# Kernel tuning notes

Hardware: AMD Instinct MI355X
Metric: run time of the kernel (lower is better)

Reference implementation:

```python
import jax, jax.numpy as jnp
import numpy as np

DIM = 128
HEADS = 4
DH = 32
SCALE = DH ** -0.5


def _ln(x, g, b):
    m = x.mean(-1, keepdims=True)
    v = x.var(-1, keepdims=True)
    return (x - m) / jnp.sqrt(v + 1e-5) * g + b


def setup_inputs() -> dict:
    key = jax.random.key(0)
    ks = jax.random.split(key, 16)
    B, N, H, W, HK, WK = 2, 6, 48, 48, 24, 24
    d, hd = DIM, HEADS * DH
    p = lambda k, s: (jax.random.normal(k, s, jnp.float32) * 0.02)
    return {
        "q": jax.random.normal(ks[0], (B, N, d, H, W), jnp.float32),
        "k": jax.random.normal(ks[1], (B, N, d, HK, WK), jnp.float32),
        "v": jax.random.normal(ks[2], (B, N, d, HK, WK), jnp.float32),
        "skip": jax.random.normal(ks[3], (B, d, H, W), jnp.float32),
        "lnq_g": jnp.ones(d), "lnq_b": jnp.zeros(d),
        "Wq": p(ks[4], (d, hd)), "bq": jnp.zeros(hd),
        "lnk_g": jnp.ones(d), "lnk_b": jnp.zeros(d),
        "Wk": p(ks[5], (d, hd)), "bk": jnp.zeros(hd),
        "lnv_g": jnp.ones(d), "lnv_b": jnp.zeros(d),
        "Wv": p(ks[6], (d, hd)), "bv": jnp.zeros(hd),
        "Wp": p(ks[7], (hd, d)), "bp": jnp.zeros(d),
        "pre_g": jnp.ones(d), "pre_b": jnp.zeros(d),
        "W1": p(ks[8], (d, 2 * d)), "b1": jnp.zeros(2 * d),
        "W2": p(ks[9], (2 * d, d)), "b2": jnp.zeros(d),
        "post_g": jnp.ones(d), "post_b": jnp.zeros(d),
    }


def reference(q, k, v, skip, lnq_g, lnq_b, Wq, bq, lnk_g, lnk_b, Wk, bk,
              lnv_g, lnv_b, Wv, bv, Wp, bp, pre_g, pre_b, W1, b1, W2, b2,
              post_g, post_b):
    B, N, d, H, W = q.shape
    _, _, _, HK, WK = k.shape
    Q, K = H * W, HK * WK
    # b n d H W -> b n (H W) d
    qx = q.transpose(0, 1, 3, 4, 2).reshape(B, N, Q, d)
    kx = k.transpose(0, 1, 3, 4, 2).reshape(B, N, K, d)
    vx = v.transpose(0, 1, 3, 4, 2).reshape(B, N * K, d)
    # norm + linear projections
    qp = _ln(qx, lnq_g, lnq_b) @ Wq + bq  # (B,N,Q,HEADS*DH)
    kp = _ln(kx, lnk_g, lnk_b) @ Wk + bk
    vp = _ln(vx, lnv_g, lnv_b) @ Wv + bv  # (B,N*K,HEADS*DH)
    # split heads: b ... (m d) -> (b m) ... d
    qp = qp.reshape(B, N, Q, HEADS, DH).transpose(0, 3, 1, 2, 4).reshape(B * HEADS, N, Q, DH)
    kp = kp.reshape(B, N, K, HEADS, DH).transpose(0, 3, 1, 2, 4).reshape(B * HEADS, N, K, DH)
    vp = vp.reshape(B, N * K, HEADS, DH).transpose(0, 2, 1, 3).reshape(B * HEADS, N * K, DH)
    # per-view scores, then softmax jointly over (n K)
    scores = SCALE * jnp.einsum('bnqd,bnkd->bnqk', qp, kp)
    scores = scores.transpose(0, 2, 1, 3).reshape(B * HEADS, Q, N * K)
    a = jax.nn.softmax(scores, axis=-1)
    out = jnp.einsum('bqk,bkd->bqd', a, vp)  # (B*HEADS, Q, DH)
    # merge heads: (b m) Q d -> b Q (m d)
    z = out.reshape(B, HEADS, Q, DH).transpose(0, 2, 1, 3).reshape(B, Q, HEADS * DH)
    z = z @ Wp + bp
    z = z + skip.transpose(0, 2, 3, 1).reshape(B, Q, d)
    z = _ln(z, pre_g, pre_b)
    z = z + (jax.nn.gelu(z @ W1 + b1, approximate=False) @ W2 + b2)
    z = _ln(z, post_g, post_b)
    return z.reshape(B, H, W, d).transpose(0, 3, 1, 2)
```

## Files before the change

### kernel.cpp

```cpp
#include <hip/hip_runtime.h>
#include <cmath>

#define B_    2
#define N_    6
#define D_    128
#define Q_    2304
#define K_    576
#define NK_   3456
#define HEADS_ 4
#define DH_   32
#define SCALE_ 0.17677669529663687f

typedef __attribute__((ext_vector_type(8))) short bf16x8;
typedef __attribute__((ext_vector_type(4))) float f32x4;

#if defined(__has_builtin)
#if __has_builtin(__builtin_amdgcn_cvt_pk_bf16_f32)
#define HAS_PK_BF16 1
#endif
#endif

static __device__ __forceinline__ unsigned short f2bf(float f) {
  union { float f; unsigned u; } x; x.f = f;
  unsigned u = x.u + 0x7fffu + ((x.u >> 16) & 1u);
  return (unsigned short)(u >> 16);
}
static __device__ __forceinline__ unsigned pkbf(float a, float b) {
#ifdef HAS_PK_BF16
  typedef __attribute__((ext_vector_type(2))) __bf16 vbf2;
  union { vbf2 v; unsigned u; } cv;
  cv.v = __builtin_amdgcn_cvt_pk_bf16_f32(a, b);
  return cv.u;
#else
  return (unsigned)f2bf(a) | ((unsigned)f2bf(b) << 16);
#endif
}

__global__ __launch_bounds__(256) void k_prep_wt(
    const float* __restrict__ Wq, const float* __restrict__ Wk,
    const float* __restrict__ Wv, const float* __restrict__ Wp,
    const float* __restrict__ W1, const float* __restrict__ W2,
    unsigned short* __restrict__ WTq, unsigned short* __restrict__ WTk,
    unsigned short* __restrict__ WTv, unsigned short* __restrict__ WTp,
    unsigned short* __restrict__ WT1, unsigned short* __restrict__ WT2)
{
  __shared__ float tile[32][33];
  const int wb = blockIdx.x, t = threadIdx.x;
  const float* src; unsigned short* dst; int Kd, J, tl;
  if      (wb < 16) { src = Wq; dst = WTq; Kd = 128; J = 128; tl = wb; }
  else if (wb < 32) { src = Wk; dst = WTk; Kd = 128; J = 128; tl = wb - 16; }
  else if (wb < 48) { src = Wv; dst = WTv; Kd = 128; J = 128; tl = wb - 32; }
  else if (wb < 64) { src = Wp; dst = WTp; Kd = 128; J = 128; tl = wb - 48; }
  else if (wb < 96) { src = W1; dst = WT1; Kd = 128; J = 256; tl = wb - 64; }
  else              { src = W2; dst = WT2; Kd = 256; J = 128; tl = wb - 96; }
  const int njt = J >> 5;
  const int tj = tl % njt, tk = tl / njt;
#pragma unroll
  for (int i = 0; i < 4; ++i) {
    int idx = t + 256 * i;
    int r = idx >> 5, c = idx & 31;
    tile[r][c] = src[(size_t)(tk * 32 + r) * J + tj * 32 + c];
  }
  __syncthreads();
#pragma unroll
  for (int i = 0; i < 2; ++i) {
    int idx = t + 256 * i;
    int rr = idx >> 4, c2 = (idx & 15) << 1;
    *(unsigned*)&dst[(size_t)(tj * 32 + rr) * Kd + tk * 32 + c2] =
        pkbf(tile[c2][rr], tile[c2 + 1][rr]);
  }
}

__global__ __launch_bounds__(256) void k_ln_proj_all(
    const float* __restrict__ qin, const float* __restrict__ kin,
    const float* __restrict__ vin,
    const float* __restrict__ lnq_g, const float* __restrict__ lnq_b,
    const float* __restrict__ lnk_g, const float* __restrict__ lnk_b,
    const float* __restrict__ lnv_g, const float* __restrict__ lnv_b,
    const unsigned short* __restrict__ WTq, const unsigned short* __restrict__ WTk,
    const unsigned short* __restrict__ WTv,
    const float* __restrict__ bq, const float* __restrict__ bk,
    const float* __restrict__ bv,
    unsigned short* __restrict__ QPh, unsigned short* __restrict__ KPh,
    unsigned short* __restrict__ VPTh)
{
  __shared__ float xs[32][132];
  __shared__ unsigned short xh[32][136];
  __shared__ float gs[128], bs[128];
  __shared__ float mu[32], rsd[32];
  const int t = threadIdx.x;
  const int bid = blockIdx.x;

  const float* x; const unsigned short* WT; const float* g; const float* bl;
  const float* bias; int S, blk, mode; float osc;
  if (bid < 864)       { mode = 0; blk = bid;        x = qin; WT = WTq; g = lnq_g; bl = lnq_b; bias = bq; S = Q_; osc = SCALE_; }
  else if (bid < 1080) { mode = 0; blk = bid - 864;  x = kin; WT = WTk; g = lnk_g; bl = lnk_b; bias = bk; S = K_; osc = 1.0f; }
  else                 { mode = 1; blk = bid - 1080; x = vin; WT = WTv; g = lnv_g; bl = lnv_b; bias = bv; S = K_; osc = 1.0f; }
  const int ntile = S >> 5;
  const int o  = blk / ntile;
  const int s0 = (blk % ntile) << 5;

  if (t < 128) { gs[t] = g[t]; bs[t] = bl[t]; }
  const float* xb = x + (size_t)o * 128 * (size_t)S + s0;
#pragma unroll
  for (int i = 0; i < 4; ++i) {
    int idx = t + 256 * i;
    int c = idx >> 3, s4 = (idx & 7) << 2;
    float4 xv = *(const float4*)&xb[(size_t)c * S + s4];
    xs[s4 + 0][c] = xv.x; xs[s4 + 1][c] = xv.y;
    xs[s4 + 2][c] = xv.z; xs[s4 + 3][c] = xv.w;
  }
  __syncthreads();
  {
    int s = t >> 3, l8 = t & 7;
    float sum = 0.f, sq = 0.f;
    for (int c = l8; c < 128; c += 8) { float v = xs[s][c]; sum += v; sq += v * v; }
#pragma unroll
    for (int off = 4; off > 0; off >>= 1) {
      sum += __shfl_down(sum, off, 8);
      sq  += __shfl_down(sq,  off, 8);
    }
    if (l8 == 0) {
      float mth = sum * 0.0078125f;
      float var = sq * 0.0078125f - mth * mth;
      mu[s] = mth; rsd[s] = rsqrtf(var + 1e-5f);
    }
  }
  __syncthreads();
#pragma unroll
  for (int i = 0; i < 8; ++i) {
    int idx = t + 256 * i;
    int s = idx >> 6, c2 = (idx & 63) << 1;
    float y0 = (xs[s][c2]     - mu[s]) * rsd[s] * gs[c2]     + bs[c2];
    float y1 = (xs[s][c2 + 1] - mu[s]) * rsd[s] * gs[c2 + 1] + bs[c2 + 1];
    *(unsigned*)&xh[s][c2] = pkbf(y0, y1);
  }
  __syncthreads();
  const int w = t >> 6, lane = t & 63, quad = lane >> 4, l16 = lane & 15;
  const f32x4 zf = {0.f, 0.f, 0.f, 0.f};
  f32x4 acc[2][2] = {{zf, zf}, {zf, zf}};
#pragma unroll
  for (int kc = 0; kc < 4; ++kc) {
    bf16x8 a0 = *(const bf16x8*)&xh[l16][kc * 32 + quad * 8];
    bf16x8 a1 = *(const bf16x8*)&xh[16 + l16][kc * 32 + quad * 8];
    bf16x8 b0 = *(const bf16x8*)&WT[(size_t)(w * 32 + l16) * 128 + kc * 32 + quad * 8];
    bf16x8 b1 = *(const bf16x8*)&WT[(size_t)(w * 32 + 16 + l16) * 128 + kc * 32 + quad * 8];
    acc[0][0] = __builtin_amdgcn_mfma_f32_16x16x32_bf16(a0, b0, acc[0][0], 0, 0, 0);
    acc[0][1] = __builtin_amdgcn_mfma_f32_16x16x32_bf16(a0, b1, acc[0][1], 0, 0, 0);
    acc[1][0] = __builtin_amdgcn_mfma_f32_16x16x32_bf16(a1, b0, acc[1][0], 0, 0, 0);
    acc[1][1] = __builtin_amdgcn_mfma_f32_16x16x32_bf16(a1, b1, acc[1][1], 0, 0, 0);
  }
  if (mode == 0) {
    unsigned short* outh = (bid < 864) ? QPh : KPh;
    __syncthreads();
#pragma unroll
    for (int mt = 0; mt < 2; ++mt)
#pragma unroll
      for (int nt = 0; nt < 2; ++nt) {
        int col = w * 32 + nt * 16 + l16;
        float bc = bias[col];
#pragma unroll
        for (int r = 0; r < 4; ++r)
          xh[mt * 16 + quad * 4 + r][col] = f2bf((acc[mt][nt][r] + bc) * osc);
      }
    __syncthreads();
#pragma unroll
    for (int i = 0; i < 2; ++i) {
      int s = i * 16 + (t >> 4), c8 = (t & 15) << 3;
      *(uint4*)&outh[((size_t)o * S + s0 + s) * 128 + c8] = *(uint4*)&xh[s][c8];
    }
  } else {
    const int b = o / 6, n = o % 6;
#pragma unroll
    for (int mt = 0; mt < 2; ++mt)
#pragma unroll
      for (int nt = 0; nt < 2; ++nt) {
        int col = w * 32 + nt * 16 + l16;
        int hh = col >> 5, dh = col & 31;
        float bc = bias[col];
        ushort4 pk;
        *(unsigned*)&pk.x = pkbf(acc[mt][nt][0] + bc, acc[mt][nt][1] + bc);
        *(unsigned*)&pk.z = pkbf(acc[mt][nt][2] + bc, acc[mt][nt][3] + bc);
        int s = n * 576 + s0 + mt * 16 + quad * 4;
        *(ushort4*)&VPTh[((size_t)(b * 4 + hh) * 32 + dh) * (size_t)NK_ + s] = pk;
      }
  }
}

__global__ __launch_bounds__(256) void k_attn_mfma(
    const unsigned short* __restrict__ QPh, const unsigned short* __restrict__ KPh,
    const unsigned short* __restrict__ VPTh, float* __restrict__ PO,
    float* __restrict__ Pl)
{
  __shared__ __align__(16) char smem_u[10240];
  unsigned short (*plds)[2][16][40] = (unsigned short (*)[2][16][40])smem_u;
  float (*ol)[16][32] = (float (*)[16][32])smem_u;
  __shared__ float ll[4][2][4][16];
  const int t = threadIdx.x;
  const int w = t >> 6, lane = t & 63;
  const int quad = lane >> 4, l16 = lane & 15;
  const int qt = blockIdx.x % 72;
  const int rest = blockIdx.x / 72;
  const int bhx = rest >> 1, ks = rest & 1;
  const int bb = bhx >> 2, h = bhx & 3;
  const int q0 = qt << 5;

  const unsigned short* vbase = VPTh + (size_t)bhx * 32 * (size_t)NK_;
  const f32x4 zf = {0.f, 0.f, 0.f, 0.f};
  f32x4 o00 = zf, o01 = zf, o10 = zf, o11 = zf;
  float lsum0 = 0.f, lsum1 = 0.f;

  const int m8 = ks * 4 + w;
  int c0 = (108 * m8) >> 3, c1 = (108 * (m8 + 1)) >> 3;

  while (c0 < c1) {
    const int nn = c0 / 18;
    const int cend = min(c1, (nn + 1) * 18);
    const unsigned short* kb = &KPh[((size_t)(bb * 6 + nn) * K_) * 128 + h * 32];
    const unsigned short* qb = &QPh[((size_t)(bb * 6 + nn) * Q_ + q0) * 128 + h * 32];
    bf16x8 qc0 = *(const bf16x8*)&qb[(size_t)l16 * 128 + quad * 8];
    bf16x8 qc1 = *(const bf16x8*)&qb[(size_t)(16 + l16) * 128 + quad * 8];

    int kl = (c0 - nn * 18) << 5;
    bf16x8 kf0 = *(const bf16x8*)&kb[(size_t)(kl + l16) * 128 + quad * 8];
    bf16x8 kf1 = *(const bf16x8*)&kb[(size_t)(kl + 16 + l16) * 128 + quad * 8];
    const unsigned short* vb = vbase + ((size_t)c0 << 5);
    bf16x8 vf0 = *(const bf16x8*)&vb[(size_t)l16 * NK_ + quad * 8];
    bf16x8 vf1 = *(const bf16x8*)&vb[(size_t)(16 + l16) * NK_ + quad * 8];

    for (int kc = c0; kc < cend; ++kc) {
      const int kln = (kc + 1 - nn * 18) << 5;
      bf16x8 nk0 = *(const bf16x8*)&kb[(size_t)(kln + l16) * 128 + quad * 8];
      bf16x8 nk1 = *(const bf16x8*)&kb[(size_t)(kln + 16 + l16) * 128 + quad * 8];
      const unsigned short* vbn = vbase + ((size_t)(kc + 1) << 5);
      bf16x8 nv0 = *(const bf16x8*)&vbn[(size_t)l16 * NK_ + quad * 8];
      bf16x8 nv1 = *(const bf16x8*)&vbn[(size_t)(16 + l16) * NK_ + quad * 8];

      f32x4 s00 = __builtin_amdgcn_mfma_f32_16x16x32_bf16(kf0, qc0, zf, 0, 0, 0);
      f32x4 s01 = __builtin_amdgcn_mfma_f32_16x16x32_bf16(kf1, qc0, zf, 0, 0, 0);
      f32x4 s10 = __builtin_amdgcn_mfma_f32_16x16x32_bf16(kf0, qc1, zf, 0, 0, 0);
      f32x4 s11 = __builtin_amdgcn_mfma_f32_16x16x32_bf16(kf1, qc1, zf, 0, 0, 0);

      float a00 = __expf(fminf(s00.x, 70.f)), a01 = __expf(fminf(s00.y, 70.f));
      float a02 = __expf(fminf(s00.z, 70.f)), a03 = __expf(fminf(s00.w, 70.f));
      float a10 = __expf(fminf(s01.x, 70.f)), a11 = __expf(fminf(s01.y, 70.f));
      float a12 = __expf(fminf(s01.z, 70.f)), a13 = __expf(fminf(s01.w, 70.f));
      lsum0 += (a00 + a01 + a02 + a03) + (a10 + a11 + a12 + a13);
      float b00 = __expf(fminf(s10.x, 70.f)), b01 = __expf(fminf(s10.y, 70.f));
      float b02 = __expf(fminf(s10.z, 70.f)), b03 = __expf(fminf(s10.w, 70.f));
      float b10 = __expf(fminf(s11.x, 70.f)), b11 = __expf(fminf(s11.y, 70.f));
      float b12 = __expf(fminf(s11.z, 70.f)), b13 = __expf(fminf(s11.w, 70.f));
      lsum1 += (b00 + b01 + b02 + b03) + (b10 + b11 + b12 + b13);

      uint2 w0a; w0a.x = pkbf(a00, a01); w0a.y = pkbf(a02, a03);
      uint2 w0b; w0b.x = pkbf(a10, a11); w0b.y = pkbf(a12, a13);
      uint2 w1a; w1a.x = pkbf(b00, b01); w1a.y = pkbf(b02, b03);
      uint2 w1b; w1b.x = pkbf(b10, b11); w1b.y = pkbf(b12, b13);
      *(uint2*)&plds[w][0][l16][quad * 4]      = w0a;
      *(uint2*)&plds[w][0][l16][16 + quad * 4] = w0b;
      *(uint2*)&plds[w][1][l16][quad * 4]      = w1a;
      *(uint2*)&plds[w][1][l16][16 + quad * 4] = w1b;
      bf16x8 pf0 = *(const bf16x8*)&plds[w][0][l16][quad * 8];
      bf16x8 pf1 = *(const bf16x8*)&plds[w][1][l16][quad * 8];

      o00 = __builtin_amdgcn_mfma_f32_16x16x32_bf16(pf0, vf0, o00, 0, 0, 0);
      o01 = __builtin_amdgcn_mfma_f32_16x16x32_bf16(pf0, vf1, o01, 0, 0, 0);
      o10 = __builtin_amdgcn_mfma_f32_16x16x32_bf16(pf1, vf0, o10, 0, 0, 0);
      o11 = __builtin_amdgcn_mfma_f32_16x16x32_bf16(pf1, vf1, o11, 0, 0, 0);

      kf0 = nk0; kf1 = nk1; vf0 = nv0; vf1 = nv1;
    }
    c0 = cend;
  }

  ll[w][0][quad][l16] = lsum0;
  ll[w][1][quad][l16] = lsum1;
#pragma unroll
  for (int tt = 0; tt < 2; ++tt) {
    __syncthreads();
    f32x4 t0 = tt ? o10 : o00;
    f32x4 t1 = tt ? o11 : o01;
#pragma unroll
    for (int r = 0; r < 4; ++r) {
      ol[w][quad * 4 + r][l16]      = t0[r];
      ol[w][quad * 4 + r][16 + l16] = t1[r];
    }
    __syncthreads();
    const int q = t >> 4, i16 = t & 15, dd = i16 << 1;
    float a0 = 0.f, a1 = 0.f;
#pragma unroll
    for (int ww = 0; ww < 4; ++ww) { a0 += ol[ww][q][dd]; a1 += ol[ww][q][dd + 1]; }
    float2 r2; r2.x = a0; r2.y = a1;
    *(float2*)&PO[(((size_t)ks * 8 + bhx) * Q_ + q0 + tt * 16 + q) * 32 + dd] = r2;
    if (i16 == 0) {
      float l = 0.f;
#pragma unroll
      for (int ww = 0; ww < 4; ++ww)
#pragma unroll
        for (int qq = 0; qq < 4; ++qq) l += ll[ww][tt][qq][q];
      Pl[((size_t)ks * 8 + bhx) * Q_ + q0 + tt * 16 + q] = l;
    }
  }
}

__global__ __launch_bounds__(512) void k_tail(
    const float* __restrict__ PO, const float* __restrict__ Pl,
    const unsigned short* __restrict__ WTp, const float* __restrict__ bp,
    const float* __restrict__ skip,
    const float* __restrict__ pre_g, const float* __restrict__ pre_b,
    const unsigned short* __restrict__ WT1, const float* __restrict__ b1,
    const unsigned short* __restrict__ WT2, const float* __restrict__ b2,
    const float* __restrict__ post_g, const float* __restrict__ post_b,
    float* __restrict__ out)
{
  __shared__ float xs[16][132];
  __shared__ unsigned short xh[16][136];
  __shared__ unsigned short hb[16][264];
  __shared__ float g1s[128], b1s[128], g2s[128], b2s[128];
  __shared__ float mu[16], rsd[16];
  const int t = threadIdx.x;
  const int row0 = blockIdx.x << 4;
  const int bb = row0 / Q_, hw0 = row0 % Q_;
  const int w = t >> 6, lane = t & 63, quad = lane >> 4, l16 = lane & 15;
  const f32x4 zf = {0.f, 0.f, 0.f, 0.f};

  if (t < 128) { g1s[t] = pre_g[t]; b1s[t] = pre_b[t]; g2s[t] = post_g[t]; b2s[t] = post_b[t]; }
#pragma unroll
  for (int i = 0; i < 2; ++i) {
    int idx = t + 512 * i;
    int s = idx >> 6, c2 = (idx & 63) << 1;
    int q = hw0 + s;
    int h = c2 >> 5, dh = c2 & 31;
    size_t bq = (size_t)(bb * 4 + h) * Q_ + q;
    size_t i0 = bq * 32 + dh;
    float2 p0 = *(const float2*)&PO[i0];
    float2 p1 = *(const float2*)&PO[589824 + i0];
    float inv = 1.f / (Pl[bq] + Pl[18432 + bq]);
    *(unsigned*)&xh[s][c2] = pkbf((p0.x + p1.x) * inv, (p0.y + p1.y) * inv);
  }
  __syncthreads();
  {
    f32x4 acc = zf;
    const int col = w * 16 + l16;
#pragma unroll
    for (int kc = 0; kc < 4; ++kc) {
      bf16x8 a0 = *(const bf16x8*)&xh[l16][kc * 32 + quad * 8];
      bf16x8 b0 = *(const bf16x8*)&WTp[(size_t)col * 128 + kc * 32 + quad * 8];
      acc = __builtin_amdgcn_mfma_f32_16x16x32_bf16(a0, b0, acc, 0, 0, 0);
    }
    float bc = bp[col];
    float4 sk = *(const float4*)&skip[((size_t)bb * 128 + col) * Q_ + hw0 + quad * 4];
    xs[quad * 4 + 0][col] = acc[0] + bc + sk.x;
    xs[quad * 4 + 1][col] = acc[1] + bc + sk.y;
    xs[quad * 4 + 2][col] = acc[2] + bc + sk.z;
    xs[quad * 4 + 3][col] = acc[3] + bc + sk.w;
  }
  __syncthreads();
  {
    int s = t >> 5, lg = t & 31;
    float sum = 0.f, sq = 0.f;
    for (int c = lg; c < 128; c += 32) { float v = xs[s][c]; sum += v; sq += v * v; }
#pragma unroll
    for (int off = 16; off > 0; off >>= 1) {
      sum += __shfl_down(sum, off, 32);
      sq  += __shfl_down(sq,  off, 32);
    }
    if (lg == 0) {
      float mth = sum * 0.0078125f;
      float var = sq * 0.0078125f - mth * mth;
      mu[s] = mth; rsd[s] = rsqrtf(var + 1e-5f);
    }
  }
  __syncthreads();
#pragma unroll
  for (int i = 0; i < 2; ++i) {
    int idx = t + 512 * i;
    int s = idx >> 6, c2 = (idx & 63) << 1;
    float y0 = (xs[s][c2]     - mu[s]) * rsd[s] * g1s[c2]     + b1s[c2];
    float y1 = (xs[s][c2 + 1] - mu[s]) * rsd[s] * g1s[c2 + 1] + b1s[c2 + 1];
    xs[s][c2] = y0; xs[s][c2 + 1] = y1;
    *(unsigned*)&xh[s][c2] = pkbf(y0, y1);
  }
  __syncthreads();
  {
#pragma unroll
    for (int nt = 0; nt < 2; ++nt) {
      const int col = w * 32 + nt * 16 + l16;
      f32x4 acc = zf;
#pragma unroll
      for (int kc = 0; kc < 4; ++kc) {
        bf16x8 a0 = *(const bf16x8*)&xh[l16][kc * 32 + quad * 8];
        bf16x8 b0 = *(const bf16x8*)&WT1[(size_t)col * 128 + kc * 32 + quad * 8];
        acc = __builtin_amdgcn_mfma_f32_16x16x32_bf16(a0, b0, acc, 0, 0, 0);
      }
      float bc = b1[col];
#pragma unroll
      for (int r = 0; r < 4; ++r) {
        float hx = acc[r] + bc;
        hb[quad * 4 + r][col] =
            f2bf(0.5f * hx * (1.f + erff(hx * 0.7071067811865476f)));
      }
    }
  }
  __syncthreads();
  {
    f32x4 acc = zf;
    const int col = w * 16 + l16;
#pragma unroll
    for (int kc = 0; kc < 8; ++kc) {
      bf16x8 a0 = *(const bf16x8*)&hb[l16][kc * 32 + quad * 8];
      bf16x8 b0 = *(const bf16x8*)&WT2[(size_t)col * 256 + kc * 32 + quad * 8];
      acc = __builtin_amdgcn_mfma_f32_16x16x32_bf16(a0, b0, acc, 0, 0, 0);
    }
    float bc = b2[col];
#pragma unroll
    for (int r = 0; r < 4; ++r) {
      int row = quad * 4 + r;
      xs[row][col] = acc[r] + bc + xs[row][col];
    }
  }
  __syncthreads();
  {
    int s = t >> 5, lg = t & 31;
    float sum = 0.f, sq = 0.f;
    for (int c = lg; c < 128; c += 32) { float v = xs[s][c]; sum += v; sq += v * v; }
#pragma unroll
    for (int off = 16; off > 0; off >>= 1) {
      sum += __shfl_down(sum, off, 32);
      sq  += __shfl_down(sq,  off, 32);
    }
    if (lg == 0) {
      float mth = sum * 0.0078125f;
      float var = sq * 0.0078125f - mth * mth;
      mu[s] = mth; rsd[s] = rsqrtf(var + 1e-5f);
    }
  }
  __syncthreads();
#pragma unroll
  for (int i = 0; i < 4; ++i) {
    int idx = t + 512 * i;
    int s = idx & 15, c = idx >> 4;
    out[(size_t)bb * (128 * (size_t)Q_) + (size_t)c * Q_ + hw0 + s] =
        (xs[s][c] - mu[s]) * rsd[s] * g2s[c] + b2s[c];
  }
}

extern "C" void kernel_launch(void* const* d_in, const int* in_sizes, int n_in,
                              void* d_out, int out_size, void* d_ws, size_t ws_size,
                              hipStream_t stream) {
  const float* q     = (const float*)d_in[0];
  const float* k     = (const float*)d_in[1];
  const float* v     = (const float*)d_in[2];
  const float* skip  = (const float*)d_in[3];
  const float* lnq_g = (const float*)d_in[4];
  const float* lnq_b = (const float*)d_in[5];
  const float* Wq    = (const float*)d_in[6];
  const float* bq    = (const float*)d_in[7];
  const float* lnk_g = (const float*)d_in[8];
  const float* lnk_b = (const float*)d_in[9];
  const float* Wk    = (const float*)d_in[10];
  const float* bk    = (const float*)d_in[11];
  const float* lnv_g = (const float*)d_in[12];
  const float* lnv_b = (const float*)d_in[13];
  const float* Wv    = (const float*)d_in[14];
  const float* bvv   = (const float*)d_in[15];
  const float* Wp    = (const float*)d_in[16];
  const float* bp    = (const float*)d_in[17];
  const float* pre_g = (const float*)d_in[18];
  const float* pre_b = (const float*)d_in[19];
  const float* W1    = (const float*)d_in[20];
  const float* b1    = (const float*)d_in[21];
  const float* W2    = (const float*)d_in[22];
  const float* b2    = (const float*)d_in[23];
  const float* post_g= (const float*)d_in[24];
  const float* post_b= (const float*)d_in[25];
  float* out = (float*)d_out;

  unsigned short* QPh  = (unsigned short*)d_ws;
  unsigned short* KPh  = QPh + 3538944;
  unsigned short* VPTh = KPh + 884736;
  float* PO  = (float*)(VPTh + 884736);
  float* Pl  = PO + 1179648;
  unsigned short* WTq = (unsigned short*)(Pl + 36864);
  unsigned short* WTk = WTq + 16384;
  unsigned short* WTv = WTk + 16384;
  unsigned short* WTp = WTv + 16384;
  unsigned short* WT1 = WTp + 16384;
  unsigned short* WT2 = WT1 + 32768;

  k_prep_wt<<<dim3(128), dim3(256), 0, stream>>>(Wq, Wk, Wv, Wp, W1, W2,
                                                 WTq, WTk, WTv, WTp, WT1, WT2);
  k_ln_proj_all<<<dim3(1296), dim3(256), 0, stream>>>(
      q, k, v, lnq_g, lnq_b, lnk_g, lnk_b, lnv_g, lnv_b,
      WTq, WTk, WTv, bq, bk, bvv, QPh, KPh, VPTh);
  k_attn_mfma<<<dim3(1152), dim3(256), 0, stream>>>(QPh, KPh, VPTh, PO, Pl);
  k_tail<<<dim3(288), dim3(512), 0, stream>>>(PO, Pl, WTp, bp, skip,
                                              pre_g, pre_b, WT1, b1, WT2, b2,
                                              post_g, post_b, out);
}
```

Before: 176.9 us.

## Merge four kernels into one cooperative persistent kernel with grid syncs

Replaces the four separate launches (weight prep, LN+projection, attention, tail) with a single cooperative persistent kernel. Each phase loops over its former block indices with a grid stride, and phases are separated by grid-wide syncs. The aim is to remove launch overhead and the gaps between kernels. The exp is also folded into exp2 with a pre-scaled log2e factor on Q. Costs include grid-sync latency, occupancy capped by the 256-thread blocks and shared LDS, and the tail phase now running at 256 threads instead of 512.

```diff
diff --git a/kernel.cpp b/kernel.cpp
--- a/kernel.cpp
+++ b/kernel.cpp
@@ -1,5 +1,8 @@
 #include <hip/hip_runtime.h>
+#include <hip/hip_cooperative_groups.h>
 #include <cmath>
+
+namespace cg = cooperative_groups;
 
 #define B_    2
 #define N_    6
@@ -10,6 +13,7 @@
 #define HEADS_ 4
 #define DH_   32
 #define SCALE_ 0.17677669529663687f
+#define SCLOG2E_ 0.25504672615621814f
 
 typedef __attribute__((ext_vector_type(8))) short bf16x8;
 typedef __attribute__((ext_vector_type(4))) float f32x4;
@@ -36,445 +40,441 @@
 #endif
 }
 
-__global__ __launch_bounds__(256) void k_prep_wt(
-    const float* __restrict__ Wq, const float* __restrict__ Wk,
-    const float* __restrict__ Wv, const float* __restrict__ Wp,
-    const float* __restrict__ W1, const float* __restrict__ W2,
-    unsigned short* __restrict__ WTq, unsigned short* __restrict__ WTk,
-    unsigned short* __restrict__ WTv, unsigned short* __restrict__ WTp,
-    unsigned short* __restrict__ WT1, unsigned short* __restrict__ WT2)
+struct KArgs {
+  const float *q, *k, *v, *skip;
+  const float *lnq_g, *lnq_b, *lnk_g, *lnk_b, *lnv_g, *lnv_b;
+  const float *Wq, *bq, *Wk, *bk, *Wv, *bv;
+  const float *Wp, *bp, *pre_g, *pre_b, *W1, *b1, *W2, *b2, *post_g, *post_b;
+  unsigned short *QPh, *KPh, *VPTh;
+  unsigned short *WTq, *WTk, *WTv, *WTp, *WT1, *WT2;
+  float *PO, *Pl, *out;
+};
+
+__global__ __launch_bounds__(256, 5) void k_mega(KArgs a)
 {
-  __shared__ float tile[32][33];
-  const int wb = blockIdx.x, t = threadIdx.x;
-  const float* src; unsigned short* dst; int Kd, J, tl;
-  if      (wb < 16) { src = Wq; dst = WTq; Kd = 128; J = 128; tl = wb; }
-  else if (wb < 32) { src = Wk; dst = WTk; Kd = 128; J = 128; tl = wb - 16; }
-  else if (wb < 48) { src = Wv; dst = WTv; Kd = 128; J = 128; tl = wb - 32; }
-  else if (wb < 64) { src = Wp; dst = WTp; Kd = 128; J = 128; tl = wb - 48; }
-  else if (wb < 96) { src = W1; dst = WT1; Kd = 128; J = 256; tl = wb - 64; }
-  else              { src = W2; dst = WT2; Kd = 256; J = 128; tl = wb - 96; }
-  const int njt = J >> 5;
-  const int tj = tl % njt, tk = tl / njt;
-#pragma unroll
-  for (int i = 0; i < 4; ++i) {
-    int idx = t + 256 * i;
-    int r = idx >> 5, c = idx & 31;
-    tile[r][c] = src[(size_t)(tk * 32 + r) * J + tj * 32 + c];
-  }
-  __syncthreads();
-#pragma unroll
-  for (int i = 0; i < 2; ++i) {
-    int idx = t + 256 * i;
-    int rr = idx >> 4, c2 = (idx & 15) << 1;
-    *(unsigned*)&dst[(size_t)(tj * 32 + rr) * Kd + tk * 32 + c2] =
-        pkbf(tile[c2][rr], tile[c2 + 1][rr]);
-  }
-}
-
-__global__ __launch_bounds__(256) void k_ln_proj_all(
-    const float* __restrict__ qin, const float* __restrict__ kin,
-    const float* __restrict__ vin,
-    const float* __restrict__ lnq_g, const float* __restrict__ lnq_b,
-    const float* __restrict__ lnk_g, const float* __restrict__ lnk_b,
-    const float* __restrict__ lnv_g, const float* __restrict__ lnv_b,
-    const unsigned short* __restrict__ WTq, const unsigned short* __restrict__ WTk,
-    const unsigned short* __restrict__ WTv,
-    const float* __restrict__ bq, const float* __restrict__ bk,
-    const float* __restrict__ bv,
-    unsigned short* __restrict__ QPh, unsigned short* __restrict__ KPh,
-    unsigned short* __restrict__ VPTh)
-{
-  __shared__ float xs[32][132];
-  __shared__ unsigned short xh[32][136];
-  __shared__ float gs[128], bs[128];
-  __shared__ float mu[32], rsd[32];
+  __shared__ __align__(16) char smem[26880];
   const int t = threadIdx.x;
   const int bid = blockIdx.x;
-
-  const float* x; const unsigned short* WT; const float* g; const float* bl;
-  const float* bias; int S, blk, mode; float osc;
-  if (bid < 864)       { mode = 0; blk = bid;        x = qin; WT = WTq; g = lnq_g; bl = lnq_b; bias = bq; S = Q_; osc = SCALE_; }
-  else if (bid < 1080) { mode = 0; blk = bid - 864;  x = kin; WT = WTk; g = lnk_g; bl = lnk_b; bias = bk; S = K_; osc = 1.0f; }
-  else                 { mode = 1; blk = bid - 1080; x = vin; WT = WTv; g = lnv_g; bl = lnv_b; bias = bv; S = K_; osc = 1.0f; }
-  const int ntile = S >> 5;
-  const int o  = blk / ntile;
-  const int s0 = (blk % ntile) << 5;
-
-  if (t < 128) { gs[t] = g[t]; bs[t] = bl[t]; }
-  const float* xb = x + (size_t)o * 128 * (size_t)S + s0;
-#pragma unroll
-  for (int i = 0; i < 4; ++i) {
-    int idx = t + 256 * i;
-    int c = idx >> 3, s4 = (idx & 7) << 2;
-    float4 xv = *(const float4*)&xb[(size_t)c * S + s4];
-    xs[s4 + 0][c] = xv.x; xs[s4 + 1][c] = xv.y;
-    xs[s4 + 2][c] = xv.z; xs[s4 + 3][c] = xv.w;
-  }
-  __syncthreads();
+  const int gsz = gridDim.x;
+  const int w = t >> 6, lane = t & 63, quad = lane >> 4, l16 = lane & 15;
+  const f32x4 zf = {0.f, 0.f, 0.f, 0.f};
+
   {
-    int s = t >> 3, l8 = t & 7;
-    float sum = 0.f, sq = 0.f;
-    for (int c = l8; c < 128; c += 8) { float v = xs[s][c]; sum += v; sq += v * v; }
-#pragma unroll
-    for (int off = 4; off > 0; off >>= 1) {
-      sum += __shfl_down(sum, off, 8);
-      sq  += __shfl_down(sq,  off, 8);
-    }
-    if (l8 == 0) {
-      float mth = sum * 0.0078125f;
-      float var = sq * 0.0078125f - mth * mth;
-      mu[s] = mth; rsd[s] = rsqrtf(var + 1e-5f);
+    float (*tile)[33] = (float (*)[33])smem;
+    for (int wb = bid; wb < 128; wb += gsz) {
+      const float* src; unsigned short* dst; int Kd, J, tl;
+      if      (wb < 16) { src = a.Wq; dst = a.WTq; Kd = 128; J = 128; tl = wb; }
+      else if (wb < 32) { src = a.Wk; dst = a.WTk; Kd = 128; J = 128; tl = wb - 16; }
+      else if (wb < 48) { src = a.Wv; dst = a.WTv; Kd = 128; J = 128; tl = wb - 32; }
+      else if (wb < 64) { src = a.Wp; dst = a.WTp; Kd = 128; J = 128; tl = wb - 48; }
+      else if (wb < 96) { src = a.W1; dst = a.WT1; Kd = 128; J = 256; tl = wb - 64; }
+      else              { src = a.W2; dst = a.WT2; Kd = 256; J = 128; tl = wb - 96; }
+      const int njt = J >> 5;
+      const int tj = tl % njt, tk = tl / njt;
+#pragma unroll
+      for (int i = 0; i < 4; ++i) {
+        int idx = t + 256 * i;
+        int r = idx >> 5, c = idx & 31;
+        tile[r][c] = src[(size_t)(tk * 32 + r) * J + tj * 32 + c];
+      }
+      __syncthreads();
+#pragma unroll
+      for (int i = 0; i < 2; ++i) {
+        int idx = t + 256 * i;
+        int rr = idx >> 4, c2 = (idx & 15) << 1;
+        *(unsigned*)&dst[(size_t)(tj * 32 + rr) * Kd + tk * 32 + c2] =
+            pkbf(tile[c2][rr], tile[c2 + 1][rr]);
+      }
+      __syncthreads();
     }
   }
-  __syncthreads();
-#pragma unroll
-  for (int i = 0; i < 8; ++i) {
-    int idx = t + 256 * i;
-    int s = idx >> 6, c2 = (idx & 63) << 1;
-    float y0 = (xs[s][c2]     - mu[s]) * rsd[s] * gs[c2]     + bs[c2];
-    float y1 = (xs[s][c2 + 1] - mu[s]) * rsd[s] * gs[c2 + 1] + bs[c2 + 1];
-    *(unsigned*)&xh[s][c2] = pkbf(y0, y1);
+  cg::this_grid().sync();
+
+  {
+    float (*xs)[132] = (float (*)[132])smem;
+    unsigned short (*xh)[136] = (unsigned short (*)[136])(smem + 16896);
+    float* gs  = (float*)(smem + 25600);
+    float* bs  = (float*)(smem + 26112);
+    float* mu  = (float*)(smem + 26624);
+    float* rsd = (float*)(smem + 26752);
+    for (int tl = bid; tl < 1296; tl += gsz) {
+      const float* x; const unsigned short* WT; const float* g; const float* bl;
+      const float* bias; int S, blk, mode; float osc;
+      if (tl < 864)       { mode = 0; blk = tl;        x = a.q; WT = a.WTq; g = a.lnq_g; bl = a.lnq_b; bias = a.bq; S = Q_; osc = SCLOG2E_; }
+      else if (tl < 1080) { mode = 0; blk = tl - 864;  x = a.k; WT = a.WTk; g = a.lnk_g; bl = a.lnk_b; bias = a.bk; S = K_; osc = 1.0f; }
+      else                { mode = 1; blk = tl - 1080; x = a.v; WT = a.WTv; g = a.lnv_g; bl = a.lnv_b; bias = a.bv; S = K_; osc = 1.0f; }
+      const int ntile = S >> 5;
+      const int o  = blk / ntile;
+      const int s0 = (blk % ntile) << 5;
+
+      if (t < 128) { gs[t] = g[t]; bs[t] = bl[t]; }
+      const float* xb = x + (size_t)o * 128 * (size_t)S + s0;
+#pragma unroll
+      for (int i = 0; i < 4; ++i) {
+        int idx = t + 256 * i;
+        int c = idx >> 3, s4 = (idx & 7) << 2;
+        float4 xv = *(const float4*)&xb[(size_t)c * S + s4];
+        xs[s4 + 0][c] = xv.x; xs[s4 + 1][c] = xv.y;
+        xs[s4 + 2][c] = xv.z; xs[s4 + 3][c] = xv.w;
+      }
+      __syncthreads();
+      {
+        int s = t >> 3, l8 = t & 7;
+        float sum = 0.f, sq = 0.f;
+        for (int c = l8; c < 128; c += 8) { float v = xs[s][c]; sum += v; sq += v * v; }
+#pragma unroll
+        for (int off = 4; off > 0; off >>= 1) {
+          sum += __shfl_down(sum, off, 8);
+          sq  += __shfl_down(sq,  off, 8);
+        }
+        if (l8 == 0) {
+          float mth = sum * 0.0078125f;
+          float var = sq * 0.0078125f - mth * mth;
+          mu[s] = mth; rsd[s] = rsqrtf(var + 1e-5f);
+        }
+      }
+      __syncthreads();
+#pragma unroll
+      for (int i = 0; i < 8; ++i) {
+        int idx = t + 256 * i;
+        int s = idx >> 6, c2 = (idx & 63) << 1;
+        float y0 = (xs[s][c2]     - mu[s]) * rsd[s] * gs[c2]     + bs[c2];
+        float y1 = (xs[s][c2 + 1] - mu[s]) * rsd[s] * gs[c2 + 1] + bs[c2 + 1];
+        *(unsigned*)&xh[s][c2] = pkbf(y0, y1);
+      }
+      __syncthreads();
+      f32x4 acc[2][2] = {{zf, zf}, {zf, zf}};
+#pragma unroll
+      for (int kc = 0; kc < 4; ++kc) {
+        bf16x8 a0 = *(const bf16x8*)&xh[l16][kc * 32 + quad * 8];
+        bf16x8 a1 = *(const bf16x8*)&xh[16 + l16][kc * 32 + quad * 8];
+        bf16x8 b0 = *(const bf16x8*)&WT[(size_t)(w * 32 + l16) * 128 + kc * 32 + quad * 8];
+        bf16x8 b1 = *(const bf16x8*)&WT[(size_t)(w * 32 + 16 + l16) * 128 + kc * 32 + quad * 8];
+        acc[0][0] = __builtin_amdgcn_mfma_f32_16x16x32_bf16(a0, b0, acc[0][0], 0, 0, 0);
+        acc[0][1] = __builtin_amdgcn_mfma_f32_16x16x32_bf16(a0, b1, acc[0][1], 0, 0, 0);
+        acc[1][0] = __builtin_amdgcn_mfma_f32_16x16x32_bf16(a1, b0, acc[1][0], 0, 0, 0);
+        acc[1][1] = __builtin_amdgcn_mfma_f32_16x16x32_bf16(a1, b1, acc[1][1], 0, 0, 0);
+      }
+      if (mode == 0) {
+        unsigned short* outh = (tl < 864) ? a.QPh : a.KPh;
+        __syncthreads();
+#pragma unroll
+        for (int mt = 0; mt < 2; ++mt)
+#pragma unroll
+          for (int nt = 0; nt < 2; ++nt) {
+            int col = w * 32 + nt * 16 + l16;
+            float bc = bias[col];
+#pragma unroll
+            for (int r = 0; r < 4; ++r)
+              xh[mt * 16 + quad * 4 + r][col] = f2bf((acc[mt][nt][r] + bc) * osc);
+          }
+        __syncthreads();
+#pragma unroll
+        for (int i = 0; i < 2; ++i) {
+          int s = i * 16 + (t >> 4), c8 = (t & 15) << 3;
+          *(uint4*)&outh[((size_t)o * S + s0 + s) * 128 + c8] = *(uint4*)&xh[s][c8];
+        }
+      } else {
+        const int b = o / 6, n = o % 6;
+#pragma unroll
+        for (int mt = 0; mt < 2; ++mt)
+#pragma unroll
+          for (int nt = 0; nt < 2; ++nt) {
+            int col = w * 32 + nt * 16 + l16;
+            int hh = col >> 5, dh = col & 31;
+            float bc = bias[col];
+            ushort4 pk;
+            *(unsigned*)&pk.x = pkbf(acc[mt][nt][0] + bc, acc[mt][nt][1] + bc);
+            *(unsigned*)&pk.z = pkbf(acc[mt][nt][2] + bc, acc[mt][nt][3] + bc);
+            int s = n * 576 + s0 + mt * 16 + quad * 4;
+            *(ushort4*)&a.VPTh[((size_t)(b * 4 + hh) * 32 + dh) * (size_t)NK_ + s] = pk;
+          }
+      }
+      __syncthreads();
+    }
   }
-  __syncthreads();
-  const int w = t >> 6, lane = t & 63, quad = lane >> 4, l16 = lane & 15;
-  const f32x4 zf = {0.f, 0.f, 0.f, 0.f};
-  f32x4 acc[2][2] = {{zf, zf}, {zf, zf}};
-#pragma unroll
-  for (int kc = 0; kc < 4; ++kc) {
-    bf16x8 a0 = *(const bf16x8*)&xh[l16][kc * 32 + quad * 8];
-    bf16x8 a1 = *(const bf16x8*)&xh[16 + l16][kc * 32 + quad * 8];
-    bf16x8 b0 = *(const bf16x8*)&WT[(size_t)(w * 32 + l16) * 128 + kc * 32 + quad * 8];
-    bf16x8 b1 = *(const bf16x8*)&WT[(size_t)(w * 32 + 16 + l16) * 128 + kc * 32 + quad * 8];
-    acc[0][0] = __builtin_amdgcn_mfma_f32_16x16x32_bf16(a0, b0, acc[0][0], 0, 0, 0);
-    acc[0][1] = __builtin_amdgcn_mfma_f32_16x16x32_bf16(a0, b1, acc[0][1], 0, 0, 0);
-    acc[1][0] = __builtin_amdgcn_mfma_f32_16x16x32_bf16(a1, b0, acc[1][0], 0, 0, 0);
-    acc[1][1] = __builtin_amdgcn_mfma_f32_16x16x32_bf16(a1, b1, acc[1][1], 0, 0, 0);
+  cg::this_grid().sync();
+
+  {
+    unsigned short (*plds)[2][16][40] = (unsigned short (*)[2][16][40])smem;
+    float (*ol)[16][32] = (float (*)[16][32])smem;
+    float (*ll)[2][4][16] = (float (*)[2][4][16])(smem + 10240);
+    for (int ab = bid; ab < 1152; ab += gsz) {
+      const int qt = ab % 72;
+      const int rest = ab / 72;
+      const int bhx = rest >> 1, ks = rest & 1;
+      const int bb = bhx >> 2, h = bhx & 3;
+      const int q0 = qt << 5;
+
+      const unsigned short* vbase = a.VPTh + (size_t)bhx * 32 * (size_t)NK_;
+      f32x4 o00 = zf, o01 = zf, o10 = zf, o11 = zf;
+      float lsum0 = 0.f, lsum1 = 0.f;
+
+      const int m8 = ks * 4 + w;
+      int c0 = (108 * m8) >> 3, c1 = (108 * (m8 + 1)) >> 3;
+
+      while (c0 < c1) {
+        const int nn = c0 / 18;
+        const int cend = min(c1, (nn + 1) * 18);
+        const unsigned short* kb = &a.KPh[((size_t)(bb * 6 + nn) * K_) * 128 + h * 32];
+        const unsigned short* qb = &a.QPh[((size_t)(bb * 6 + nn) * Q_ + q0) * 128 + h * 32];
+        bf16x8 qc0 = *(const bf16x8*)&qb[(size_t)l16 * 128 + quad * 8];
+        bf16x8 qc1 = *(const bf16x8*)&qb[(size_t)(16 + l16) * 128 + quad * 8];
+
+        int kl = (c0 - nn * 18) << 5;
+        bf16x8 kf0 = *(const bf16x8*)&kb[(size_t)(kl + l16) * 128 + quad * 8];
+        bf16x8 kf1 = *(const bf16x8*)&kb[(size_t)(kl + 16 + l16) * 128 + quad * 8];
+        const unsigned short* vb = vbase + ((size_t)c0 << 5);
+        bf16x8 vf0 = *(const bf16x8*)&vb[(size_t)l16 * NK_ + quad * 8];
+        bf16x8 vf1 = *(const bf16x8*)&vb[(size_t)(16 + l16) * NK_ + quad * 8];
+
+        for (int kc = c0; kc < cend; ++kc) {
+          const int kln = (kc + 1 - nn * 18) << 5;
+          bf16x8 nk0 = *(const bf16x8*)&kb[(size_t)(kln + l16) * 128 + quad * 8];
+          bf16x8 nk1 = *(const bf16x8*)&kb[(size_t)(kln + 16 + l16) * 128 + quad * 8];
+          const unsigned short* vbn = vbase + ((size_t)(kc + 1) << 5);
+          bf16x8 nv0 = *(const bf16x8*)&vbn[(size_t)l16 * NK_ + quad * 8];
+          bf16x8 nv1 = *(const bf16x8*)&vbn[(size_t)(16 + l16) * NK_ + quad * 8];
+
+          f32x4 s00 = __builtin_amdgcn_mfma_f32_16x16x32_bf16(kf0, qc0, zf, 0, 0, 0);
+          f32x4 s01 = __builtin_amdgcn_mfma_f32_16x16x32_bf16(kf1, qc0, zf, 0, 0, 0);
+          f32x4 s10 = __builtin_amdgcn_mfma_f32_16x16x32_bf16(kf0, qc1, zf, 0, 0, 0);
+          f32x4 s11 = __builtin_amdgcn_mfma_f32_16x16x32_bf16(kf1, qc1, zf, 0, 0, 0);
+
+          float a00 = exp2f(fminf(s00.x, 100.f)), a01 = exp2f(fminf(s00.y, 100.f));
+          float a02 = exp2f(fminf(s00.z, 100.f)), a03 = exp2f(fminf(s00.w, 100.f));
+          float a10 = exp2f(fminf(s01.x, 100.f)), a11 = exp2f(fminf(s01.y, 100.f));
+          float a12 = exp2f(fminf(s01.z, 100.f)), a13 = exp2f(fminf(s01.w, 100.f));
+          lsum0 += (a00 + a01 + a02 + a03) + (a10 + a11 + a12 + a13);
+          float b00 = exp2f(fminf(s10.x, 100.f)), b01 = exp2f(fminf(s10.y, 100.f));
+          float b02 = exp2f(fminf(s10.z, 100.f)), b03 = exp2f(fminf(s10.w, 100.f));
+          float b10 = exp2f(fminf(s11.x, 100.f)), b11 = exp2f(fminf(s11.y, 100.f));
+          float b12 = exp2f(fminf(s11.z, 100.f)), b13 = exp2f(fminf(s11.w, 100.f));
+          lsum1 += (b00 + b01 + b02 + b03) + (b10 + b11 + b12 + b13);
+
+          uint2 w0a; w0a.x = pkbf(a00, a01); w0a.y = pkbf(a02, a03);
+          uint2 w0b; w0b.x = pkbf(a10, a11); w0b.y = pkbf(a12, a13);
+          uint2 w1a; w1a.x = pkbf(b00, b01); w1a.y = pkbf(b02, b03);
+          uint2 w1b; w1b.x = pkbf(b10, b11); w1b.y = pkbf(b12, b13);
+          *(uint2*)&plds[w][0][l16][quad * 4]      = w0a;
+          *(uint2*)&plds[w][0][l16][16 + quad * 4] = w0b;
+          *(uint2*)&plds[w][1][l16][quad * 4]      = w1a;
+          *(uint2*)&plds[w][1][l16][16 + quad * 4] = w1b;
+          bf16x8 pf0 = *(const bf16x8*)&plds[w][0][l16][quad * 8];
+          bf16x8 pf1 = *(const bf16x8*)&plds[w][1][l16][quad * 8];
+
+          o00 = __builtin_amdgcn_mfma_f32_16x16x32_bf16(pf0, vf0, o00, 0, 0, 0);
+          o01 = __builtin_amdgcn_mfma_f32_16x16x32_bf16(pf0, vf1, o01, 0, 0, 0);
+          o10 = __builtin_amdgcn_mfma_f32_16x16x32_bf16(pf1, vf0, o10, 0, 0, 0);
+          o11 = __builtin_amdgcn_mfma_f32_16x16x32_bf16(pf1, vf1, o11, 0, 0, 0);
+
+          kf0 = nk0; kf1 = nk1; vf0 = nv0; vf1 = nv1;
+        }
+        c0 = cend;
+      }
+
+      ll[w][0][quad][l16] = lsum0;
+      ll[w][1][quad][l16] = lsum1;
+#pragma unroll
+      for (int tt = 0; tt < 2; ++tt) {
+        __syncthreads();
+        f32x4 t0 = tt ? o10 : o00;
+        f32x4 t1 = tt ? o11 : o01;
+#pragma unroll
+        for (int r = 0; r < 4; ++r) {
+          ol[w][quad * 4 + r][l16]      = t0[r];
+          ol[w][quad * 4 + r][16 + l16] = t1[r];
+        }
+        __syncthreads();
+        const int q = t >> 4, i16 = t & 15, dd = i16 << 1;
+        float a0 = 0.f, a1 = 0.f;
+#pragma unroll
+        for (int ww = 0; ww < 4; ++ww) { a0 += ol[ww][q][dd]; a1 += ol[ww][q][dd + 1]; }
+        float2 r2; r2.x = a0; r2.y = a1;
+        *(float2*)&a.PO[(((size_t)ks * 8 + bhx) * Q_ + q0 + tt * 16 + q) * 32 + dd] = r2;
+        if (i16 == 0) {
+          float l = 0.f;
+#pragma unroll
+          for (int ww = 0; ww < 4; ++ww)
+#pragma unroll
+            for (int qq = 0; qq < 4; ++qq) l += ll[ww][tt][qq][q];
+          a.Pl[((size_t)ks * 8 + bhx) * Q_ + q0 + tt * 16 + q] = l;
+        }
+      }
+      __syncthreads();
+    }
   }
-  if (mode == 0) {
-    unsigned short* outh = (bid < 864) ? QPh : KPh;
-    __syncthreads();
-#pragma unroll
-    for (int mt = 0; mt < 2; ++mt)
+  cg::this_grid().sync();
+
+  {
+    float (*xs)[132] = (float (*)[132])smem;
+    unsigned short (*xh)[136] = (unsigned short (*)[136])(smem + 8448);
+    unsigned short (*hb)[264] = (unsigned short (*)[264])(smem + 12800);
+    float* g1s = (float*)(smem + 21248);
+    float* b1s = (float*)(smem + 21760);
+    float* g2s = (float*)(smem + 22272);
+    float* b2s = (float*)(smem + 22784);
+    float* mu  = (float*)(smem + 23296);
+    float* rsd = (float*)(smem + 23360);
+    for (int tl = bid; tl < 288; tl += gsz) {
+      const int row0 = tl << 4;
+      const int bb = row0 / Q_, hw0 = row0 % Q_;
+
+      if (t < 128) { g1s[t] = a.pre_g[t]; b1s[t] = a.pre_b[t]; g2s[t] = a.post_g[t]; b2s[t] = a.post_b[t]; }
+#pragma unroll
+      for (int i = 0; i < 4; ++i) {
+        int idx = t + 256 * i;
+        int s = idx >> 6, c2 = (idx & 63) << 1;
+        int q = hw0 + s;
+        int h = c2 >> 5, dh = c2 & 31;
+        size_t bq = (size_t)(bb * 4 + h) * Q_ + q;
+        size_t i0 = bq * 32 + dh;
+        float2 p0 = *(const float2*)&a.PO[i0];
+        float2 p1 = *(const float2*)&a.PO[589824 + i0];
+        float inv = 1.f / (a.Pl[bq] + a.Pl[18432 + bq]);
+        *(unsigned*)&xh[s][c2] = pkbf((p0.x + p1.x) * inv, (p0.y + p1.y) * inv);
+      }
+      __syncthreads();
 #pragma unroll
       for (int nt = 0; nt < 2; ++nt) {
-        int col = w * 32 + nt * 16 + l16;
-        float bc = bias[col];
-#pragma unroll
-        for (int r = 0; r < 4; ++r)
-          xh[mt * 16 + quad * 4 + r][col] = f2bf((acc[mt][nt][r] + bc) * osc);
-      }
-    __syncthreads();
-#pragma unroll
-    for (int i = 0; i < 2; ++i) {
-      int s = i * 16 + (t >> 4), c8 = (t & 15) << 3;
-      *(uint4*)&outh[((size_t)o * S + s0 + s) * 128 + c8] = *(uint4*)&xh[s][c8];
-    }
-  } else {
-    const int b = o / 6, n = o % 6;
-#pragma unroll
-    for (int mt = 0; mt < 2; ++mt)
+        const int col = w * 32 + nt * 16 + l16;
+        f32x4 acc = zf;
+#pragma unroll
+        for (int kc = 0; kc < 4; ++kc) {
+          bf16x8 a0 = *(const bf16x8*)&xh[l16][kc * 32 + quad * 8];
+          bf16x8 b0 = *(const bf16x8*)&a.WTp[(size_t)col * 128 + kc * 32 + quad * 8];
+          acc = __builtin_amdgcn_mfma_f32_16x16x32_bf16(a0, b0, acc, 0, 0, 0);
+        }
+        float bc = a.bp[col];
+        float4 sk = *(const float4*)&a.skip[((size_t)bb * 128 + col) * Q_ + hw0 + quad * 4];
+        xs[quad * 4 + 0][col] = acc[0] + bc + sk.x;
+        xs[quad * 4 + 1][col] = acc[1] + bc + sk.y;
+        xs[quad * 4 + 2][col] = acc[2] + bc + sk.z;
+        xs[quad * 4 + 3][col] = acc[3] + bc + sk.w;
+      }
+      __syncthreads();
+      {
+        int s = t >> 4, lg = t & 15;
+        float sum = 0.f, sq = 0.f;
+        for (int c = lg; c < 128; c += 16) { float v = xs[s][c]; sum += v; sq += v * v; }
+#pragma unroll
+        for (int off = 8; off > 0; off >>= 1) {
+          sum += __shfl_down(sum, off, 16);
+          sq  += __shfl_down(sq,  off, 16);
+        }
+        if (lg == 0) {
+          float mth = sum * 0.0078125f;
+          float var = sq * 0.0078125f - mth * mth;
+          mu[s] = mth; rsd[s] = rsqrtf(var + 1e-5f);
+        }
+      }
+      __syncthreads();
+#pragma unroll
+      for (int i = 0; i < 4; ++i) {
+        int idx = t + 256 * i;
+        int s = idx >> 6, c2 = (idx & 63) << 1;
+        float y0 = (xs[s][c2]     - mu[s]) * rsd[s] * g1s[c2]     + b1s[c2];
+        float y1 = (xs[s][c2 + 1] - mu[s]) * rsd[s] * g1s[c2 + 1] + b1s[c2 + 1];
+        xs[s][c2] = y0; xs[s][c2 + 1] = y1;
+        *(unsigned*)&xh[s][c2] = pkbf(y0, y1);
+      }
+      __syncthreads();
+#pragma unroll
+      for (int nt = 0; nt < 4; ++nt) {
+        const int col = w * 64 + nt * 16 + l16;
+        f32x4 acc = zf;
+#pragma unroll
+        for (int kc = 0; kc < 4; ++kc) {
+          bf16x8 a0 = *(const bf16x8*)&xh[l16][kc * 32 + quad * 8];
+          bf16x8 b0 = *(const bf16x8*)&a.WT1[(size_t)col * 128 + kc * 32 + quad * 8];
+          acc = __builtin_amdgcn_mfma_f32_16x16x32_bf16(a0, b0, acc, 0, 0, 0);
+        }
+        float bc = a.b1[col];
+#pragma unroll
+        for (int r = 0; r < 4; ++r) {
+          float hx = acc[r] + bc;
+          hb[quad * 4 + r][col] =
+              f2bf(0.5f * hx * (1.f + erff(hx * 0.7071067811865476f)));
+        }
+      }
+      __syncthreads();
 #pragma unroll
       for (int nt = 0; nt < 2; ++nt) {
-        int col = w * 32 + nt * 16 + l16;
-        int hh = col >> 5, dh = col & 31;
-        float bc = bias[col];
-        ushort4 pk;
-        *(unsigned*)&pk.x = pkbf(acc[mt][nt][0] + bc, acc[mt][nt][1] + bc);
-        *(unsigned*)&pk.z = pkbf(acc[mt][nt][2] + bc, acc[mt][nt][3] + bc);
-        int s = n * 576 + s0 + mt * 16 + quad * 4;
-        *(ushort4*)&VPTh[((size_t)(b * 4 + hh) * 32 + dh) * (size_t)NK_ + s] = pk;
-      }
-  }
-}
-
-__global__ __launch_bounds__(256) void k_attn_mfma(
-    const unsigned short* __restrict__ QPh, const unsigned short* __restrict__ KPh,
-    const unsigned short* __restrict__ VPTh, float* __restrict__ PO,
-    float* __restrict__ Pl)
-{
-  __shared__ __align__(16) char smem_u[10240];
-  unsigned short (*plds)[2][16][40] = (unsigned short (*)[2][16][40])smem_u;
-  float (*ol)[16][32] = (float (*)[16][32])smem_u;
-  __shared__ float ll[4][2][4][16];
-  const int t = threadIdx.x;
-  const int w = t >> 6, lane = t & 63;
-  const int quad = lane >> 4, l16 = lane & 15;
-  const int qt = blockIdx.x % 72;
-  const int rest = blockIdx.x / 72;
-  const int bhx = rest >> 1, ks = rest & 1;
-  const int bb = bhx >> 2, h = bhx & 3;
-  const int q0 = qt << 5;
-
-  const unsigned short* vbase = VPTh + (size_t)bhx * 32 * (size_t)NK_;
-  const f32x4 zf = {0.f, 0.f, 0.f, 0.f};
-  f32x4 o00 = zf, o01 = zf, o10 = zf, o11 = zf;
-  float lsum0 = 0.f, lsum1 = 0.f;
-
-  const int m8 = ks * 4 + w;
-  int c0 = (108 * m8) >> 3, c1 = (108 * (m8 + 1)) >> 3;
-
-  while (c0 < c1) {
-    const int nn = c0 / 18;
-    const int cend = min(c1, (nn + 1) * 18);
-    const unsigned short* kb = &KPh[((size_t)(bb * 6 + nn) * K_) * 128 + h * 32];
-    const unsigned short* qb = &QPh[((size_t)(bb * 6 + nn) * Q_ + q0) * 128 + h * 32];
-    bf16x8 qc0 = *(const bf16x8*)&qb[(size_t)l16 * 128 + quad * 8];
-    bf16x8 qc1 = *(const bf16x8*)&qb[(size_t)(16 + l16) * 128 + quad * 8];
-
-    int kl = (c0 - nn * 18) << 5;
-    bf16x8 kf0 = *(const bf16x8*)&kb[(size_t)(kl + l16) * 128 + quad * 8];
-    bf16x8 kf1 = *(const bf16x8*)&kb[(size_t)(kl + 16 + l16) * 128 + quad * 8];
-    const unsigned short* vb = vbase + ((size_t)c0 << 5);
-    bf16x8 vf0 = *(const bf16x8*)&vb[(size_t)l16 * NK_ + quad * 8];
-    bf16x8 vf1 = *(const bf16x8*)&vb[(size_t)(16 + l16) * NK_ + quad * 8];
-
-    for (int kc = c0; kc < cend; ++kc) {
-      const int kln = (kc + 1 - nn * 18) << 5;
-      bf16x8 nk0 = *(const bf16x8*)&kb[(size_t)(kln + l16) * 128 + quad * 8];
-      bf16x8 nk1 = *(const bf16x8*)&kb[(size_t)(kln + 16 + l16) * 128 + quad * 8];
-      const unsigned short* vbn = vbase + ((size_t)(kc + 1) << 5);
-      bf16x8 nv0 = *(const bf16x8*)&vbn[(size_t)l16 * NK_ + quad * 8];
-      bf16x8 nv1 = *(const bf16x8*)&vbn[(size_t)(16 + l16) * NK_ + quad * 8];
-
-      f32x4 s00 = __builtin_amdgcn_mfma_f32_16x16x32_bf16(kf0, qc0, zf, 0, 0, 0);
-      f32x4 s01 = __builtin_amdgcn_mfma_f32_16x16x32_bf16(kf1, qc0, zf, 0, 0, 0);
-      f32x4 s10 = __builtin_amdgcn_mfma_f32_16x16x32_bf16(kf0, qc1, zf, 0, 0, 0);
-      f32x4 s11 = __builtin_amdgcn_mfma_f32_16x16x32_bf16(kf1, qc1, zf, 0, 0, 0);
-
-      float a00 = __expf(fminf(s00.x, 70.f)), a01 = __expf(fminf(s00.y, 70.f));
-      float a02 = __expf(fminf(s00.z, 70.f)), a03 = __expf(fminf(s00.w, 70.f));
-      float a10 = __expf(fminf(s01.x, 70.f)), a11 = __expf(fminf(s01.y, 70.f));
-      float a12 = __expf(fminf(s01.z, 70.f)), a13 = __expf(fminf(s01.w, 70.f));
-      lsum0 += (a00 + a01 + a02 + a03) + (a10 + a11 + a12 + a13);
-      float b00 = __expf(fminf(s10.x, 70.f)), b01 = __expf(fminf(s10.y, 70.f));
-      float b02 = __expf(fminf(s10.z, 70.f)), b03 = __expf(fminf(s10.w, 70.f));
-      float b10 = __expf(fminf(s11.x, 70.f)), b11 = __expf(fminf(s11.y, 70.f));
-      float b12 = __expf(fminf(s11.z, 70.f)), b13 = __expf(fminf(s11.w, 70.f));
-      lsum1 += (b00 + b01 + b02 + b03) + (b10 + b11 + b12 + b13);
-
-      uint2 w0a; w0a.x = pkbf(a00, a01); w0a.y = pkbf(a02, a03);
-      uint2 w0b; w0b.x = pkbf(a10, a11); w0b.y = pkbf(a12, a13);
-      uint2 w1a; w1a.x = pkbf(b00, b01); w1a.y = pkbf(b02, b03);
-      uint2 w1b; w1b.x = pkbf(b10, b11); w1b.y = pkbf(b12, b13);
-      *(uint2*)&plds[w][0][l16][quad * 4]      = w0a;
-      *(uint2*)&plds[w][0][l16][16 + quad * 4] = w0b;
-      *(uint2*)&plds[w][1][l16][quad * 4]      = w1a;
-      *(uint2*)&plds[w][1][l16][16 + quad * 4] = w1b;
-      bf16x8 pf0 = *(const bf16x8*)&plds[w][0][l16][quad * 8];
-      bf16x8 pf1 = *(const bf16x8*)&plds[w][1][l16][quad * 8];
-
-      o00 = __builtin_amdgcn_mfma_f32_16x16x32_bf16(pf0, vf0, o00, 0, 0, 0);
-      o01 = __builtin_amdgcn_mfma_f32_16x16x32_bf16(pf0, vf1, o01, 0, 0, 0);
-      o10 = __builtin_amdgcn_mfma_f32_16x16x32_bf16(pf1, vf0, o10, 0, 0, 0);
-      o11 = __builtin_amdgcn_mfma_f32_16x16x32_bf16(pf1, vf1, o11, 0, 0, 0);
-
-      kf0 = nk0; kf1 = nk1; vf0 = nv0; vf1 = nv1;
-    }
-    c0 = cend;
-  }
-
-  ll[w][0][quad][l16] = lsum0;
-  ll[w][1][quad][l16] = lsum1;
-#pragma unroll
-  for (int tt = 0; tt < 2; ++tt) {
-    __syncthreads();
-    f32x4 t0 = tt ? o10 : o00;
-    f32x4 t1 = tt ? o11 : o01;
-#pragma unroll
-    for (int r = 0; r < 4; ++r) {
-      ol[w][quad * 4 + r][l16]      = t0[r];
-      ol[w][quad * 4 + r][16 + l16] = t1[r];
-    }
-    __syncthreads();
-    const int q = t >> 4, i16 = t & 15, dd = i16 << 1;
-    float a0 = 0.f, a1 = 0.f;
-#pragma unroll
-    for (int ww = 0; ww < 4; ++ww) { a0 += ol[ww][q][dd]; a1 += ol[ww][q][dd + 1]; }
-    float2 r2; r2.x = a0; r2.y = a1;
-    *(float2*)&PO[(((size_t)ks * 8 + bhx) * Q_ + q0 + tt * 16 + q) * 32 + dd] = r2;
-    if (i16 == 0) {
-      float l = 0.f;
-#pragma unroll
-      for (int ww = 0; ww < 4; ++ww)
-#pragma unroll
-        for (int qq = 0; qq < 4; ++qq) l += ll[ww][tt][qq][q];
-      Pl[((size_t)ks * 8 + bhx) * Q_ + q0 + tt * 16 + q] = l;
+        const int col = w * 32 + nt * 16 + l16;
+        f32x4 acc = zf;
+#pragma unroll
+        for (int kc = 0; kc < 8; ++kc) {
+          bf16x8 a0 = *(const bf16x8*)&hb[l16][kc * 32 + quad * 8];
+          bf16x8 b0 = *(const bf16x8*)&a.WT2[(size_t)col * 256 + kc * 32 + quad * 8];
+          acc = __builtin_amdgcn_mfma_f32_16x16x32_bf16(a0, b0, acc, 0, 0, 0);
+        }
+        float bc = a.b2[col];
+#pragma unroll
+        for (int r = 0; r < 4; ++r) {
+          int row = quad * 4 + r;
+          xs[row][col] = acc[r] + bc + xs[row][col];
+        }
+      }
+      __syncthreads();
+      {
+        int s = t >> 4, lg = t & 15;
+        float sum = 0.f, sq = 0.f;
+        for (int c = lg; c < 128; c += 16) { float v = xs[s][c]; sum += v; sq += v * v; }
+#pragma unroll
+        for (int off = 8; off > 0; off >>= 1) {
+          sum += __shfl_down(sum, off, 16);
+          sq  += __shfl_down(sq,  off, 16);
+        }
+        if (lg == 0) {
+          float mth = sum * 0.0078125f;
+          float var = sq * 0.0078125f - mth * mth;
+          mu[s] = mth; rsd[s] = rsqrtf(var + 1e-5f);
+        }
+      }
+      __syncthreads();
+#pragma unroll
+      for (int i = 0; i < 8; ++i) {
+        int idx = t + 256 * i;
+        int s = idx & 15, c = idx >> 4;
+        a.out[(size_t)bb * (128 * (size_t)Q_) + (size_t)c * Q_ + hw0 + s] =
+            (xs[s][c] - mu[s]) * rsd[s] * g2s[c] + b2s[c];
+      }
+      __syncthreads();
     }
   }
 }
 
-__global__ __launch_bounds__(512) void k_tail(
-    const float* __restrict__ PO, const float* __restrict__ Pl,
-    const unsigned short* __restrict__ WTp, const float* __restrict__ bp,
-    const float* __restrict__ skip,
-    const float* __restrict__ pre_g, const float* __restrict__ pre_b,
-    const unsigned short* __restrict__ WT1, const float* __restrict__ b1,
-    const unsigned short* __restrict__ WT2, const float* __restrict__ b2,
-    const float* __restrict__ post_g, const float* __restrict__ post_b,
-    float* __restrict__ out)
-{
-  __shared__ float xs[16][132];
-  __shared__ unsigned short xh[16][136];
-  __shared__ unsigned short hb[16][264];
-  __shared__ float g1s[128], b1s[128], g2s[128], b2s[128];
-  __shared__ float mu[16], rsd[16];
-  const int t = threadIdx.x;
-  const int row0 = blockIdx.x << 4;
-  const int bb = row0 / Q_, hw0 = row0 % Q_;
-  const int w = t >> 6, lane = t & 63, quad = lane >> 4, l16 = lane & 15;
-  const f32x4 zf = {0.f, 0.f, 0.f, 0.f};
-
-  if (t < 128) { g1s[t] = pre_g[t]; b1s[t] = pre_b[t]; g2s[t] = post_g[t]; b2s[t] = post_b[t]; }
-#pragma unroll
-  for (int i = 0; i < 2; ++i) {
-    int idx = t + 512 * i;
-    int s = idx >> 6, c2 = (idx & 63) << 1;
-    int q = hw0 + s;
-    int h = c2 >> 5, dh = c2 & 31;
-    size_t bq = (size_t)(bb * 4 + h) * Q_ + q;
-    size_t i0 = bq * 32 + dh;
-    float2 p0 = *(const float2*)&PO[i0];
-    float2 p1 = *(const float2*)&PO[589824 + i0];
-    float inv = 1.f / (Pl[bq] + Pl[18432 + bq]);
-    *(unsigned*)&xh[s][c2] = pkbf((p0.x + p1.x) * inv, (p0.y + p1.y) * inv);
-  }
-  __syncthreads();
-  {
-    f32x4 acc = zf;
-    const int col = w * 16 + l16;
-#pragma unroll
-    for (int kc = 0; kc < 4; ++kc) {
-      bf16x8 a0 = *(const bf16x8*)&xh[l16][kc * 32 + quad * 8];
-      bf16x8 b0 = *(const bf16x8*)&WTp[(size_t)col * 128 + kc * 32 + quad * 8];
-      acc = __builtin_amdgcn_mfma_f32_16x16x32_bf16(a0, b0, acc, 0, 0, 0);
-    }
-    float bc = bp[col];
-    float4 sk = *(const float4*)&skip[((size_t)bb * 128 + col) * Q_ + hw0 + quad * 4];
-    xs[quad * 4 + 0][col] = acc[0] + bc + sk.x;
-    xs[quad * 4 + 1][col] = acc[1] + bc + sk.y;
-    xs[quad * 4 + 2][col] = acc[2] + bc + sk.z;
-    xs[quad * 4 + 3][col] = acc[3] + bc + sk.w;
-  }
-  __syncthreads();
-  {
-    int s = t >> 5, lg = t & 31;
-    float sum = 0.f, sq = 0.f;
-    for (int c = lg; c < 128; c += 32) { float v = xs[s][c]; sum += v; sq += v * v; }
-#pragma unroll
-    for (int off = 16; off > 0; off >>= 1) {
-      sum += __shfl_down(sum, off, 32);
-      sq  += __shfl_down(sq,  off, 32);
-    }
-    if (lg == 0) {
-      float mth = sum * 0.0078125f;
-      float var = sq * 0.0078125f - mth * mth;
-      mu[s] = mth; rsd[s] = rsqrtf(var + 1e-5f);
-    }
-  }
-  __syncthreads();
-#pragma unroll
-  for (int i = 0; i < 2; ++i) {
-    int idx = t + 512 * i;
-    int s = idx >> 6, c2 = (idx & 63) << 1;
-    float y0 = (xs[s][c2]     - mu[s]) * rsd[s] * g1s[c2]     + b1s[c2];
-    float y1 = (xs[s][c2 + 1] - mu[s]) * rsd[s] * g1s[c2 + 1] + b1s[c2 + 1];
-    xs[s][c2] = y0; xs[s][c2 + 1] = y1;
-    *(unsigned*)&xh[s][c2] = pkbf(y0, y1);
-  }
-  __syncthreads();
-  {
-#pragma unroll
-    for (int nt = 0; nt < 2; ++nt) {
-      const int col = w * 32 + nt * 16 + l16;
-      f32x4 acc = zf;
-#pragma unroll
-      for (int kc = 0; kc < 4; ++kc) {
-        bf16x8 a0 = *(const bf16x8*)&xh[l16][kc * 32 + quad * 8];
-        bf16x8 b0 = *(const bf16x8*)&WT1[(size_t)col * 128 + kc * 32 + quad * 8];
-        acc = __builtin_amdgcn_mfma_f32_16x16x32_bf16(a0, b0, acc, 0, 0, 0);
-      }
-      float bc = b1[col];
-#pragma unroll
-      for (int r = 0; r < 4; ++r) {
-        float hx = acc[r] + bc;
-        hb[quad * 4 + r][col] =
-            f2bf(0.5f * hx * (1.f + erff(hx * 0.7071067811865476f)));
-      }
-    }
-  }
-  __syncthreads();
-  {
-    f32x4 acc = zf;
-    const int col = w * 16 + l16;
-#pragma unroll
-    for (int kc = 0; kc < 8; ++kc) {
-      bf16x8 a0 = *(const bf16x8*)&hb[l16][kc * 32 + quad * 8];
-      bf16x8 b0 = *(const bf16x8*)&WT2[(size_t)col * 256 + kc * 32 + quad * 8];
-      acc = __builtin_amdgcn_mfma_f32_16x16x32_bf16(a0, b0, acc, 0, 0, 0);
-    }
-    float bc = b2[col];
-#pragma unroll
-    for (int r = 0; r < 4; ++r) {
-      int row = quad * 4 + r;
-      xs[row][col] = acc[r] + bc + xs[row][col];
-    }
-  }
-  __syncthreads();
-  {
-    int s = t >> 5, lg = t & 31;
-    float sum = 0.f, sq = 0.f;
-    for (int c = lg; c < 128; c += 32) { float v = xs[s][c]; sum += v; sq += v * v; }
-#pragma unroll
-    for (int off = 16; off > 0; off >>= 1) {
-      sum += __shfl_down(sum, off, 32);
-      sq  += __shfl_down(sq,  off, 32);
-    }
-    if (lg == 0) {
-      float mth = sum * 0.0078125f;
-      float var = sq * 0.0078125f - mth * mth;
-      mu[s] = mth; rsd[s] = rsqrtf(var + 1e-5f);
-    }
-  }
-  __syncthreads();
-#pragma unroll
-  for (int i = 0; i < 4; ++i) {
-    int idx = t + 512 * i;
-    int s = idx & 15, c = idx >> 4;
-    out[(size_t)bb * (128 * (size_t)Q_) + (size_t)c * Q_ + hw0 + s] =
-        (xs[s][c] - mu[s]) * rsd[s] * g2s[c] + b2s[c];
-  }
-}
-
 extern "C" void kernel_launch(void* const* d_in, const int* in_sizes, int n_in,
                               void* d_out, int out_size, void* d_ws, size_t ws_size,
                               hipStream_t stream) {
-  const float* q     = (const float*)d_in[0];
-  const float* k     = (const float*)d_in[1];
-  const float* v     = (const float*)d_in[2];
-  const float* skip  = (const float*)d_in[3];
-  const float* lnq_g = (const float*)d_in[4];
-  const float* lnq_b = (const float*)d_in[5];
-  const float* Wq    = (const float*)d_in[6];
-  const float* bq    = (const float*)d_in[7];
-  const float* lnk_g = (const float*)d_in[8];
-  const float* lnk_b = (const float*)d_in[9];
-  const float* Wk    = (const float*)d_in[10];
-  const float* bk    = (const float*)d_in[11];
-  const float* lnv_g = (const float*)d_in[12];
-  const float* lnv_b = (const float*)d_in[13];
-  const float* Wv    = (const float*)d_in[14];
-  const float* bvv   = (const float*)d_in[15];
-  const float* Wp    = (const float*)d_in[16];
-  const float* bp    = (const float*)d_in[17];
-  const float* pre_g = (const float*)d_in[18];
-  const float* pre_b = (const float*)d_in[19];
-  const float* W1    = (const float*)d_in[20];
-  const float* b1    = (const float*)d_in[21];
-  const float* W2    = (const float*)d_in[22];
-  const float* b2    = (const float*)d_in[23];
-  const float* post_g= (const float*)d_in[24];
-  const float* post_b= (const float*)d_in[25];
-  float* out = (float*)d_out;
+  KArgs ka;
+  ka.q     = (const float*)d_in[0];
+  ka.k     = (const float*)d_in[1];
+  ka.v     = (const float*)d_in[2];
+  ka.skip  = (const float*)d_in[3];
+  ka.lnq_g = (const float*)d_in[4];
+  ka.lnq_b = (const float*)d_in[5];
+  ka.Wq    = (const float*)d_in[6];
+  ka.bq    = (const float*)d_in[7];
+  ka.lnk_g = (const float*)d_in[8];
+  ka.lnk_b = (const float*)d_in[9];
+  ka.Wk    = (const float*)d_in[10];
+  ka.bk    = (const float*)d_in[11];
+  ka.lnv_g = (const float*)d_in[12];
+  ka.lnv_b = (const float*)d_in[13];
+  ka.Wv    = (const float*)d_in[14];
+  ka.bv    = (const float*)d_in[15];
+  ka.Wp    = (const float*)d_in[16];
+  ka.bp    = (const float*)d_in[17];
+  ka.pre_g = (const float*)d_in[18];
+  ka.pre_b = (const float*)d_in[19];
+  ka.W1    = (const float*)d_in[20];
+  ka.b1    = (const float*)d_in[21];
+  ka.W2    = (const float*)d_in[22];
+  ka.b2    = (const float*)d_in[23];
+  ka.post_g= (const float*)d_in[24];
+  ka.post_b= (const float*)d_in[25];
+  ka.out   = (float*)d_out;
 
   unsigned short* QPh  = (unsigned short*)d_ws;
   unsigned short* KPh  = QPh + 3538944;
@@ -487,14 +487,18 @@
   unsigned short* WTp = WTv + 16384;
   unsigned short* WT1 = WTp + 16384;
   unsigned short* WT2 = WT1 + 32768;
-
-  k_prep_wt<<<dim3(128), dim3(256), 0, stream>>>(Wq, Wk, Wv, Wp, W1, W2,
-                                                 WTq, WTk, WTv, WTp, WT1, WT2);
-  k_ln_proj_all<<<dim3(1296), dim3(256), 0, stream>>>(
-      q, k, v, lnq_g, lnq_b, lnk_g, lnk_b, lnv_g, lnv_b,
-      WTq, WTk, WTv, bq, bk, bvv, QPh, KPh, VPTh);
-  k_attn_mfma<<<dim3(1152), dim3(256), 0, stream>>>(QPh, KPh, VPTh, PO, Pl);
-  k_tail<<<dim3(288), dim3(512), 0, stream>>>(PO, Pl, WTp, bp, skip,
-                                              pre_g, pre_b, WT1, b1, WT2, b2,
-                                              post_g, post_b, out);
+  ka.QPh = QPh; ka.KPh = KPh; ka.VPTh = VPTh;
+  ka.PO = PO; ka.Pl = Pl;
+  ka.WTq = WTq; ka.WTk = WTk; ka.WTv = WTv;
+  ka.WTp = WTp; ka.WT1 = WT1; ka.WT2 = WT2;
+
+  int occ = 0;
+  hipOccupancyMaxActiveBlocksPerMultiprocessor(&occ, k_mega, 256, 0);
+  if (occ < 1) occ = 1;
+  long long cap = (long long)occ * 256;
+  int grid = (int)(cap < 1296 ? cap : 1296);
+
+  void* params[] = { (void*)&ka };
+  hipLaunchCooperativeKernel((const void*)k_mega, dim3(grid), dim3(256),
+                             params, 0, stream);
 }
```

Result: slower. 422.6 us (+138.8%).
